# Performance work log

Hardware: AMD Instinct MI355X
Metric: run time of the kernel (lower is better)

Reference implementation:

```python
import jax, jax.numpy as jnp
import numpy as np

NB_HEAD = 16
SIZE_PER_HEAD = 64
D_MODEL = 1024
OUT_DIM = NB_HEAD * SIZE_PER_HEAD
BIG_NEG = 1e10


def setup_inputs() -> dict:
    key = jax.random.key(0)
    ks = jax.random.split(key, 6)
    B, L = 2, 2048
    q = jax.random.normal(ks[0], (B, L, D_MODEL), dtype=jnp.float32)
    k = jax.random.normal(ks[1], (B, L, D_MODEL), dtype=jnp.float32)
    v = jax.random.normal(ks[2], (B, L, D_MODEL), dtype=jnp.float32)
    v_mask = jnp.ones((B, L), dtype=jnp.float32)
    q_mask = jnp.ones((B, L), dtype=jnp.float32)
    # glorot_normal-ish init for the three projection kernels
    std = (2.0 / (D_MODEL + OUT_DIM)) ** 0.5
    q_kernel = jax.random.normal(ks[3], (D_MODEL, OUT_DIM), dtype=jnp.float32) * std
    k_kernel = jax.random.normal(ks[4], (D_MODEL, OUT_DIM), dtype=jnp.float32) * std
    v_kernel = jax.random.normal(ks[5], (D_MODEL, OUT_DIM), dtype=jnp.float32) * std
    return {"q": q, "k": k, "v": v, "v_mask": v_mask, "q_mask": q_mask,
            "q_kernel": q_kernel, "k_kernel": k_kernel, "v_kernel": v_kernel}


def reference(q, k, v, v_mask, q_mask, q_kernel, k_kernel, v_kernel):
    B, Lq, _ = q.shape
    Lk = k.shape[1]
    H, D = NB_HEAD, SIZE_PER_HEAD
    # projections -> [B, L, H, D]
    qw = (q @ q_kernel).reshape(B, Lq, H, D)
    kw = (k @ k_kernel).reshape(B, Lk, H, D)
    vw = (v @ v_kernel).reshape(B, Lk, H, D)
    # scaled dot-product scores [B, H, Lq, Lk]
    scores = jnp.einsum('bqhd,bkhd->bhqk', qw, kw) / jnp.sqrt(jnp.float32(D))
    # additive key mask (original permutes so mask broadcasts over key axis)
    scores = scores - (1.0 - v_mask)[:, None, None, :] * BIG_NEG
    a = jax.nn.softmax(scores, axis=-1)
    # weighted sum -> [B, Lq, H, D] -> [B, Lq, H*D]
    o = jnp.einsum('bhqk,bkhd->bqhd', a, vw).reshape(B, Lq, H * D)
    # multiplicative query mask on output
    o = o * q_mask[:, :, None]
    return o
```

## Files before the change

kernel.cpp:

```cpp
#include <hip/hip_runtime.h>
#include <hip/hip_bf16.h>

#define B_SZ 2
#define SEQ  2048
#define DM   1024
#define NH   16
#define HD   64

typedef __attribute__((ext_vector_type(8))) short bf16x8;
typedef __attribute__((ext_vector_type(4))) short bf16x4;
typedef __attribute__((ext_vector_type(4))) float f32x4;
typedef __attribute__((ext_vector_type(16))) float f32x16;

__device__ __forceinline__ short f2b(float f) {
    __hip_bfloat16 h = __float2bfloat16(f);
    return *reinterpret_cast<short*>(&h);
}

__device__ __forceinline__ int cvtpk(float a, float b) {
    int r;
    asm("v_cvt_pk_bf16_f32 %0, %1, %2" : "=v"(r) : "v"(a), "v"(b));
    return r;
}

__device__ __forceinline__ void async_copy16(void* lds, const void* g) {
    __builtin_amdgcn_global_load_lds(
        (const __attribute__((address_space(1))) void*)g,
        (__attribute__((address_space(3))) void*)lds, 16, 0, 0);
}

__global__ __launch_bounds__(256) void kPre(
    const float* __restrict__ q, const float* __restrict__ k, const float* __restrict__ v,
    const float* __restrict__ w0, const float* __restrict__ w1, const float* __restrict__ w2,
    short* __restrict__ qb, short* __restrict__ kb, short* __restrict__ vb,
    short* __restrict__ t0, short* __restrict__ t1, short* __restrict__ t2) {
    int z = blockIdx.z, tid = threadIdx.x;
    if (z < 3) {
        const float* src = z == 0 ? q : (z == 1 ? k : v);
        short*       dst = z == 0 ? qb : (z == 1 ? kb : vb);
        size_t i = ((size_t)blockIdx.x * 256 + tid) * 8;
        float4 a0 = *reinterpret_cast<const float4*>(src + i);
        float4 a1 = *reinterpret_cast<const float4*>(src + i + 4);
        bf16x8 c;
        c[0] = f2b(a0.x); c[1] = f2b(a0.y); c[2] = f2b(a0.z); c[3] = f2b(a0.w);
        c[4] = f2b(a1.x); c[5] = f2b(a1.y); c[6] = f2b(a1.z); c[7] = f2b(a1.w);
        *reinterpret_cast<bf16x8*>(dst + i) = c;
    } else {
        if (blockIdx.x >= 256) return;
        const float* w = z == 3 ? w0 : (z == 4 ? w1 : w2);
        short*       t = z == 3 ? t0 : (z == 4 ? t1 : t2);
        __shared__ float tile[64][65];
        int n0 = (blockIdx.x & 15) * 64, k0 = (blockIdx.x >> 4) * 64;
        int c = tid & 63, rr = tid >> 6;
#pragma unroll
        for (int i = 0; i < 16; i++) {
            int kk = i * 4 + rr;
            tile[kk][c] = w[(size_t)(k0 + kk) * DM + n0 + c];
        }
        __syncthreads();
#pragma unroll
        for (int i = 0; i < 16; i++) {
            int nn = i * 4 + rr;
            t[(size_t)(n0 + nn) * DM + k0 + c] = f2b(tile[c][nn]);
        }
    }
}

__global__ __launch_bounds__(256) void kProj(
    const short* __restrict__ qb, const short* __restrict__ kb, const short* __restrict__ vb,
    const short* __restrict__ wtq, const short* __restrict__ wtk, const short* __restrict__ wtv,
    short* __restrict__ qw, short* __restrict__ kw, short* __restrict__ vwT) {
    int z = blockIdx.z;
    const short* A  = z == 0 ? qb : (z == 1 ? kb : vb);
    const short* Bt = z == 0 ? wtq : (z == 1 ? wtk : wtv);

    __shared__ short As[128 * 64];
    __shared__ short Bs[128 * 64];

    int tid = threadIdx.x;
    int m0 = blockIdx.y * 128, n0 = blockIdx.x * 128;
    int wv = tid >> 6, lane = tid & 63, quad = lane >> 4, ln = lane & 15;
    int rblk = (wv >> 1) * 64, cblk = (wv & 1) * 64;

    int rA = wv * 32;
    int srow = rA + (lane >> 3), scol = (lane & 7) * 8;

    f32x4 zero = {0.f, 0.f, 0.f, 0.f};
    f32x4 acc[4][4];
#pragma unroll
    for (int rt = 0; rt < 4; rt++)
#pragma unroll
        for (int ct = 0; ct < 4; ct++) acc[rt][ct] = zero;

    for (int ks = 0; ks < DM; ks += 64) {
        const short* gA = A  + (size_t)(m0 + srow) * DM + ks + scol;
        const short* gB = Bt + (size_t)(n0 + srow) * DM + ks + scol;
#pragma unroll
        for (int i = 0; i < 4; i++) {
            async_copy16(&As[(rA + i * 8) * 64], gA + (size_t)i * 8 * DM);
            async_copy16(&Bs[(rA + i * 8) * 64], gB + (size_t)i * 8 * DM);
        }
        __syncthreads();
#pragma unroll
        for (int kc = 0; kc < 2; kc++) {
            bf16x8 af[4], bfv[4];
#pragma unroll
            for (int rt = 0; rt < 4; rt++)
                af[rt] = *reinterpret_cast<bf16x8*>(&As[(rblk + rt * 16 + ln) * 64 + kc * 32 + quad * 8]);
#pragma unroll
            for (int ct = 0; ct < 4; ct++)
                bfv[ct] = *reinterpret_cast<bf16x8*>(&Bs[(cblk + ct * 16 + ln) * 64 + kc * 32 + quad * 8]);
#pragma unroll
            for (int rt = 0; rt < 4; rt++)
#pragma unroll
                for (int ct = 0; ct < 4; ct++)
                    acc[rt][ct] = __builtin_amdgcn_mfma_f32_16x16x32_bf16(
                        af[rt], bfv[ct], acc[rt][ct], 0, 0, 0);
        }
        __syncthreads();
    }

    if (z < 2) {
        short* C = z == 0 ? qw : kw;
#pragma unroll
        for (int rt = 0; rt < 4; rt++)
#pragma unroll
            for (int r = 0; r < 4; r++) {
                int row = m0 + rblk + rt * 16 + quad * 4 + r;
#pragma unroll
                for (int ct = 0; ct < 4; ct++)
                    C[(size_t)row * DM + n0 + cblk + ct * 16 + ln] = f2b(acc[rt][ct][r]);
            }
    } else {
#pragma unroll
        for (int rt = 0; rt < 4; rt++) {
            int srow0 = m0 + rblk + rt * 16 + quad * 4;
            int bb = srow0 >> 11, lk = srow0 & (SEQ - 1);
#pragma unroll
            for (int ct = 0; ct < 4; ct++) {
                int coln = n0 + cblk + ct * 16 + ln;
                int hh = coln >> 6, dd = coln & 63;
                bf16x4 pk;
                pk[0] = f2b(acc[rt][ct][0]); pk[1] = f2b(acc[rt][ct][1]);
                pk[2] = f2b(acc[rt][ct][2]); pk[3] = f2b(acc[rt][ct][3]);
                *reinterpret_cast<bf16x4*>(
                    &vwT[(((size_t)bb * NH + hh) * HD + dd) * SEQ + lk]) = pk;
            }
        }
    }
}

__global__ __launch_bounds__(256, 4) void kAttn(
    const short* __restrict__ qw, const short* __restrict__ kw, const short* __restrict__ vwT,
    const float* __restrict__ vmask, const float* __restrict__ qmask, float* __restrict__ out) {
    int b = blockIdx.z, h = blockIdx.y, lq0 = blockIdx.x * 64;
    int tid = threadIdx.x, wv = tid >> 6, lane = tid & 63;
    int l5 = lane & 31, half = lane >> 5;
    int g = wv & 1, h2 = wv >> 1;

    __shared__ short Ks[128][72];
    __shared__ short Vt[64][136];

    const short* qrow = qw + (size_t)(b * SEQ + lq0 + g * 32 + l5) * DM + h * HD;
    bf16x8 qf[4];
#pragma unroll
    for (int ki = 0; ki < 4; ki++)
        qf[ki] = *reinterpret_cast<const bf16x8*>(qrow + ki * 16 + half * 8);

    float lrow = 0.f;
    f32x16 o0, o1;
#pragma unroll
    for (int i = 0; i < 16; i++) { o0[i] = 0.f; o1[i] = 0.f; }

    int krow = tid >> 1, kcol = (tid & 1) * 32;
    int vrow = tid >> 2, vcol = (tid & 3) * 32;
    const short* kp = kw + (size_t)(b * SEQ + krow) * DM + h * HD + kcol;
    const short* vp = vwT + ((size_t)(b * NH + h) * HD + vrow) * SEQ + vcol;
    const float* vmb = vmask + b * SEQ;

    const float C1 = 0.18033688011f;
    const float C2 = 1.4426950e10f;

    bf16x8 kr[4], vr[4];
#pragma unroll
    for (int i = 0; i < 4; i++) {
        kr[i] = *reinterpret_cast<const bf16x8*>(kp + i * 8);
        vr[i] = *reinterpret_cast<const bf16x8*>(vp + i * 8);
    }

    for (int it = 0; it < SEQ / 128; it++) {
        int lk0 = it * 128;
#pragma unroll
        for (int i = 0; i < 4; i++) {
            *reinterpret_cast<bf16x8*>(&Ks[krow][kcol + i * 8]) = kr[i];
            *reinterpret_cast<bf16x8*>(&Vt[vrow][vcol + i * 8]) = vr[i];
        }
        __syncthreads();

        if (it + 1 < SEQ / 128) {
            kp += (size_t)128 * DM;
            vp += 128;
#pragma unroll
            for (int i = 0; i < 4; i++) {
                kr[i] = *reinterpret_cast<const bf16x8*>(kp + i * 8);
                vr[i] = *reinterpret_cast<const bf16x8*>(vp + i * 8);
            }
        }

        float rs = 0.f;
#pragma unroll
        for (int lt = 0; lt < 2; lt++) {
            int LT = h2 * 2 + lt;
            f32x16 s;
#pragma unroll
            for (int i = 0; i < 16; i++) s[i] = 0.f;
#pragma unroll
            for (int ki = 0; ki < 4; ki++) {
                bf16x8 kf = *reinterpret_cast<bf16x8*>(&Ks[LT * 32 + l5][ki * 16 + half * 8]);
                s = __builtin_amdgcn_mfma_f32_32x32x16_bf16(kf, qf[ki], s, 0, 0, 0);
            }

            float p[16];
#pragma unroll
            for (int g4 = 0; g4 < 4; g4++) {
                float4 mv = *reinterpret_cast<const float4*>(
                    &vmb[lk0 + LT * 32 + 8 * g4 + 4 * half]);
                float p0 = __builtin_amdgcn_exp2f(fmaf(s[4 * g4 + 0], C1, fmaf(mv.x, C2, -C2)));
                float p1 = __builtin_amdgcn_exp2f(fmaf(s[4 * g4 + 1], C1, fmaf(mv.y, C2, -C2)));
                float p2 = __builtin_amdgcn_exp2f(fmaf(s[4 * g4 + 2], C1, fmaf(mv.z, C2, -C2)));
                float p3 = __builtin_amdgcn_exp2f(fmaf(s[4 * g4 + 3], C1, fmaf(mv.w, C2, -C2)));
                rs += (p0 + p1) + (p2 + p3);
                p[4 * g4 + 0] = p0; p[4 * g4 + 1] = p1;
                p[4 * g4 + 2] = p2; p[4 * g4 + 3] = p3;
            }

            int wA = cvtpk(p[0],  p[1]),  wB = cvtpk(p[2],  p[3]);
            int wC = cvtpk(p[4],  p[5]),  wD = cvtpk(p[6],  p[7]);
            int wE = cvtpk(p[8],  p[9]),  wF = cvtpk(p[10], p[11]);
            int wG = cvtpk(p[12], p[13]), wH = cvtpk(p[14], p[15]);
            int xA = __shfl_xor(wA, 32), xB = __shfl_xor(wB, 32);
            int xC = __shfl_xor(wC, 32), xD = __shfl_xor(wD, 32);
            int xE = __shfl_xor(wE, 32), xF = __shfl_xor(wF, 32);
            int xG = __shfl_xor(wG, 32), xH = __shfl_xor(wH, 32);
            bool lo = (half == 0);
            union { int i[4]; bf16x8 v; } uA, uB;
            uA.i[0] = lo ? wA : xC; uA.i[1] = lo ? wB : xD;
            uA.i[2] = lo ? xA : wC; uA.i[3] = lo ? xB : wD;
            uB.i[0] = lo ? wE : xG; uB.i[1] = lo ? wF : xH;
            uB.i[2] = lo ? xE : wG; uB.i[3] = lo ? xF : wH;

            bf16x8 vf00 = *reinterpret_cast<bf16x8*>(&Vt[l5]     [(2 * LT) * 16 + half * 8]);
            bf16x8 vf01 = *reinterpret_cast<bf16x8*>(&Vt[32 + l5][(2 * LT) * 16 + half * 8]);
            bf16x8 vf10 = *reinterpret_cast<bf16x8*>(&Vt[l5]     [(2 * LT + 1) * 16 + half * 8]);
            bf16x8 vf11 = *reinterpret_cast<bf16x8*>(&Vt[32 + l5][(2 * LT + 1) * 16 + half * 8]);
            o0 = __builtin_amdgcn_mfma_f32_32x32x16_bf16(vf00, uA.v, o0, 0, 0, 0);
            o1 = __builtin_amdgcn_mfma_f32_32x32x16_bf16(vf01, uA.v, o1, 0, 0, 0);
            o0 = __builtin_amdgcn_mfma_f32_32x32x16_bf16(vf10, uB.v, o0, 0, 0, 0);
            o1 = __builtin_amdgcn_mfma_f32_32x32x16_bf16(vf11, uB.v, o1, 0, 0, 0);
        }

        rs += __shfl_xor(rs, 32);
        lrow += rs;
        __syncthreads();
    }

    float* cb = reinterpret_cast<float*>(&Ks[0][0]);
    float* lr = reinterpret_cast<float*>(&Vt[0][0]);
    int ci = g * 64 + lane;
    if (h2 == 1) {
#pragma unroll
        for (int i = 0; i < 16; i++) cb[ci + 128 * i]        = o0[i];
#pragma unroll
        for (int i = 0; i < 16; i++) cb[ci + 128 * (16 + i)] = o1[i];
        lr[ci] = lrow;
    }
    __syncthreads();
    if (h2 == 1) return;
#pragma unroll
    for (int i = 0; i < 16; i++) o0[i] += cb[ci + 128 * i];
#pragma unroll
    for (int i = 0; i < 16; i++) o1[i] += cb[ci + 128 * (16 + i)];
    lrow += lr[ci];

    int lq = lq0 + g * 32 + l5;
    float sc2 = (1.0f / lrow) * qmask[b * SEQ + lq];
    float* orow = out + (size_t)(b * SEQ + lq) * DM + h * HD;
#pragma unroll
    for (int g4 = 0; g4 < 4; g4++) {
        float4 st0, st1;
        st0.x = o0[4 * g4 + 0] * sc2; st0.y = o0[4 * g4 + 1] * sc2;
        st0.z = o0[4 * g4 + 2] * sc2; st0.w = o0[4 * g4 + 3] * sc2;
        st1.x = o1[4 * g4 + 0] * sc2; st1.y = o1[4 * g4 + 1] * sc2;
        st1.z = o1[4 * g4 + 2] * sc2; st1.w = o1[4 * g4 + 3] * sc2;
        *reinterpret_cast<float4*>(&orow[8 * g4 + 4 * half]) = st0;
        *reinterpret_cast<float4*>(&orow[32 + 8 * g4 + 4 * half]) = st1;
    }
}

extern "C" void kernel_launch(void* const* d_in, const int* in_sizes, int n_in,
                              void* d_out, int out_size, void* d_ws, size_t ws_size,
                              hipStream_t stream) {
    const float* q  = (const float*)d_in[0];
    const float* k  = (const float*)d_in[1];
    const float* v  = (const float*)d_in[2];
    const float* vm = (const float*)d_in[3];
    const float* qm = (const float*)d_in[4];
    const float* qk = (const float*)d_in[5];
    const float* kk = (const float*)d_in[6];
    const float* vk = (const float*)d_in[7];
    float* out = (float*)d_out;

    short* ws  = (short*)d_ws;
    short* wtq = ws;
    short* wtk = wtq + 1024 * 1024;
    short* wtv = wtk + 1024 * 1024;
    short* vb  = wtv + 1024 * 1024;
    short* qw  = vb + (size_t)4096 * 1024;
    short* kw  = qw + (size_t)4096 * 1024;
    short* vwT = kw + (size_t)4096 * 1024;
    short* qb = (short*)d_out;
    short* kb = qb + (size_t)4096 * 1024;

    kPre <<<dim3(2048, 1, 6), 256, 0, stream>>>(q, k, v, qk, kk, vk,
                                                qb, kb, vb, wtq, wtk, wtv);
    kProj<<<dim3(8, 32, 3), 256, 0, stream>>>(qb, kb, vb, wtq, wtk, wtv, qw, kw, vwT);
    kAttn<<<dim3(32, 16, 2), 256, 0, stream>>>(qw, kw, vwT, vm, qm, out);
}
```

Before: 230.4 us.

## Fuse fp32-to-bf16 activation conversion into projection GEMM loads; hoist mask loads

Drops the separate pass that converted q/k/v activations to bf16. The projection GEMM now reads fp32 activations directly, packs them to bf16 in registers and stores them to LDS, while weights still use async global-to-LDS copies. This removes a full read/write round trip of the activation tensors, but the A-tile loads become synchronous register loads that are re-read by the 8 column blocks at double the bytes. The attention kernel also preloads the key-mask values for the tile right after the barrier instead of loading them inside the softmax loop.

```diff
diff --git a/kernel.cpp b/kernel.cpp
--- a/kernel.cpp
+++ b/kernel.cpp
@@ -30,48 +30,33 @@
 }
 
 __global__ __launch_bounds__(256) void kPre(
-    const float* __restrict__ q, const float* __restrict__ k, const float* __restrict__ v,
     const float* __restrict__ w0, const float* __restrict__ w1, const float* __restrict__ w2,
-    short* __restrict__ qb, short* __restrict__ kb, short* __restrict__ vb,
     short* __restrict__ t0, short* __restrict__ t1, short* __restrict__ t2) {
     int z = blockIdx.z, tid = threadIdx.x;
-    if (z < 3) {
-        const float* src = z == 0 ? q : (z == 1 ? k : v);
-        short*       dst = z == 0 ? qb : (z == 1 ? kb : vb);
-        size_t i = ((size_t)blockIdx.x * 256 + tid) * 8;
-        float4 a0 = *reinterpret_cast<const float4*>(src + i);
-        float4 a1 = *reinterpret_cast<const float4*>(src + i + 4);
-        bf16x8 c;
-        c[0] = f2b(a0.x); c[1] = f2b(a0.y); c[2] = f2b(a0.z); c[3] = f2b(a0.w);
-        c[4] = f2b(a1.x); c[5] = f2b(a1.y); c[6] = f2b(a1.z); c[7] = f2b(a1.w);
-        *reinterpret_cast<bf16x8*>(dst + i) = c;
-    } else {
-        if (blockIdx.x >= 256) return;
-        const float* w = z == 3 ? w0 : (z == 4 ? w1 : w2);
-        short*       t = z == 3 ? t0 : (z == 4 ? t1 : t2);
-        __shared__ float tile[64][65];
-        int n0 = (blockIdx.x & 15) * 64, k0 = (blockIdx.x >> 4) * 64;
-        int c = tid & 63, rr = tid >> 6;
-#pragma unroll
-        for (int i = 0; i < 16; i++) {
-            int kk = i * 4 + rr;
-            tile[kk][c] = w[(size_t)(k0 + kk) * DM + n0 + c];
-        }
-        __syncthreads();
-#pragma unroll
-        for (int i = 0; i < 16; i++) {
-            int nn = i * 4 + rr;
-            t[(size_t)(n0 + nn) * DM + k0 + c] = f2b(tile[c][nn]);
-        }
+    const float* w = z == 0 ? w0 : (z == 1 ? w1 : w2);
+    short*       t = z == 0 ? t0 : (z == 1 ? t1 : t2);
+    __shared__ float tile[64][65];
+    int n0 = (blockIdx.x & 15) * 64, k0 = (blockIdx.x >> 4) * 64;
+    int c = tid & 63, rr = tid >> 6;
+#pragma unroll
+    for (int i = 0; i < 16; i++) {
+        int kk = i * 4 + rr;
+        tile[kk][c] = w[(size_t)(k0 + kk) * DM + n0 + c];
+    }
+    __syncthreads();
+#pragma unroll
+    for (int i = 0; i < 16; i++) {
+        int nn = i * 4 + rr;
+        t[(size_t)(n0 + nn) * DM + k0 + c] = f2b(tile[c][nn]);
     }
 }
 
 __global__ __launch_bounds__(256) void kProj(
-    const short* __restrict__ qb, const short* __restrict__ kb, const short* __restrict__ vb,
+    const float* __restrict__ qf32, const float* __restrict__ kf32, const float* __restrict__ vf32,
     const short* __restrict__ wtq, const short* __restrict__ wtk, const short* __restrict__ wtv,
     short* __restrict__ qw, short* __restrict__ kw, short* __restrict__ vwT) {
     int z = blockIdx.z;
-    const short* A  = z == 0 ? qb : (z == 1 ? kb : vb);
+    const float* Af = z == 0 ? qf32 : (z == 1 ? kf32 : vf32);
     const short* Bt = z == 0 ? wtq : (z == 1 ? wtk : wtv);
 
     __shared__ short As[128 * 64];
@@ -93,12 +78,20 @@
         for (int ct = 0; ct < 4; ct++) acc[rt][ct] = zero;
 
     for (int ks = 0; ks < DM; ks += 64) {
-        const short* gA = A  + (size_t)(m0 + srow) * DM + ks + scol;
         const short* gB = Bt + (size_t)(n0 + srow) * DM + ks + scol;
 #pragma unroll
+        for (int i = 0; i < 4; i++)
+            async_copy16(&Bs[(rA + i * 8) * 64], gB + (size_t)i * 8 * DM);
+
+        const float* gA = Af + (size_t)(m0 + srow) * DM + ks + scol;
+#pragma unroll
         for (int i = 0; i < 4; i++) {
-            async_copy16(&As[(rA + i * 8) * 64], gA + (size_t)i * 8 * DM);
-            async_copy16(&Bs[(rA + i * 8) * 64], gB + (size_t)i * 8 * DM);
+            float4 f0 = *reinterpret_cast<const float4*>(gA + (size_t)i * 8 * DM);
+            float4 f1 = *reinterpret_cast<const float4*>(gA + (size_t)i * 8 * DM + 4);
+            union { int w[4]; bf16x8 v; } u;
+            u.w[0] = cvtpk(f0.x, f0.y); u.w[1] = cvtpk(f0.z, f0.w);
+            u.w[2] = cvtpk(f1.x, f1.y); u.w[3] = cvtpk(f1.z, f1.w);
+            *reinterpret_cast<bf16x8*>(&As[(srow + i * 8) * 64 + scol]) = u.v;
         }
         __syncthreads();
 #pragma unroll
@@ -197,6 +190,14 @@
         }
         __syncthreads();
 
+        float4 mv8[2][4];
+#pragma unroll
+        for (int lt = 0; lt < 2; lt++)
+#pragma unroll
+            for (int g4 = 0; g4 < 4; g4++)
+                mv8[lt][g4] = *reinterpret_cast<const float4*>(
+                    &vmb[lk0 + (h2 * 2 + lt) * 32 + 8 * g4 + 4 * half]);
+
         if (it + 1 < SEQ / 128) {
             kp += (size_t)128 * DM;
             vp += 128;
@@ -223,8 +224,7 @@
             float p[16];
 #pragma unroll
             for (int g4 = 0; g4 < 4; g4++) {
-                float4 mv = *reinterpret_cast<const float4*>(
-                    &vmb[lk0 + LT * 32 + 8 * g4 + 4 * half]);
+                float4 mv = mv8[lt][g4];
                 float p0 = __builtin_amdgcn_exp2f(fmaf(s[4 * g4 + 0], C1, fmaf(mv.x, C2, -C2)));
                 float p1 = __builtin_amdgcn_exp2f(fmaf(s[4 * g4 + 1], C1, fmaf(mv.y, C2, -C2)));
                 float p2 = __builtin_amdgcn_exp2f(fmaf(s[4 * g4 + 2], C1, fmaf(mv.z, C2, -C2)));
@@ -314,15 +314,11 @@
     short* wtq = ws;
     short* wtk = wtq + 1024 * 1024;
     short* wtv = wtk + 1024 * 1024;
-    short* vb  = wtv + 1024 * 1024;
-    short* qw  = vb + (size_t)4096 * 1024;
+    short* qw  = wtv + 1024 * 1024;
     short* kw  = qw + (size_t)4096 * 1024;
     short* vwT = kw + (size_t)4096 * 1024;
-    short* qb = (short*)d_out;
-    short* kb = qb + (size_t)4096 * 1024;
-
-    kPre <<<dim3(2048, 1, 6), 256, 0, stream>>>(q, k, v, qk, kk, vk,
-                                                qb, kb, vb, wtq, wtk, wtv);
-    kProj<<<dim3(8, 32, 3), 256, 0, stream>>>(qb, kb, vb, wtq, wtk, wtv, qw, kw, vwT);
+
+    kPre <<<dim3(256, 1, 3), 256, 0, stream>>>(qk, kk, vk, wtq, wtk, wtv);
+    kProj<<<dim3(8, 32, 3), 256, 0, stream>>>(q, k, v, wtq, wtk, wtv, qw, kw, vwT);
     kAttn<<<dim3(32, 16, 2), 256, 0, stream>>>(qw, kw, vwT, vm, qm, out);
 }
```

Measured after the change: 238.9 us. 3.7% more time.
